# Optimization experiments

Measured on AMD Instinct MI355X. Metric: run time of the kernel, lower is better.

## Reference

```python
import jax, jax.numpy as jnp
import numpy as np

EPS = 1e-5
H = 1024  # hidden_size
IN = 1024  # input_size
B = 4096


def _layer_norm(x, gamma, beta):
    mu = jnp.mean(x, axis=-1, keepdims=True)
    var = jnp.mean(jnp.square(x - mu), axis=-1, keepdims=True)
    return (x - mu) * jax.lax.rsqrt(var + EPS) * gamma + beta


def setup_inputs() -> dict:
    key = jax.random.key(0)
    ks = jax.random.split(key, 8)
    s_h = 1.0 / np.sqrt(H)
    s_x = 1.0 / np.sqrt(IN)
    return {
        "x": jax.random.normal(ks[0], (B, IN), dtype=jnp.float32),
        "h": jax.random.normal(ks[1], (B, H), dtype=jnp.float32),
        "c": jax.random.normal(ks[2], (B, H), dtype=jnp.float32),
        # hidden_lin: Linear(H, 4H) with bias; input_lin: Linear(IN, 4H) no bias
        "W_h": jax.random.uniform(ks[3], (H, 4 * H), jnp.float32, -s_h, s_h),
        "b_h": jax.random.uniform(ks[4], (4 * H,), jnp.float32, -s_h, s_h),
        "W_x": jax.random.uniform(ks[5], (IN, 4 * H), jnp.float32, -s_x, s_x),
        # 4 gate LayerNorms stacked [4,H], plus LayerNorm for c
        "ln_g": jnp.ones((4, H), jnp.float32),
        "ln_b": jnp.zeros((4, H), jnp.float32),
        "lnc_g": jnp.ones((H,), jnp.float32),
        "lnc_b": jnp.zeros((H,), jnp.float32),
    }


def reference(x, h, c, W_h, b_h, W_x, ln_g, ln_b, lnc_g, lnc_b):
    # ifgo = hidden_lin(h) + input_lin(x) : [B, 4H]
    ifgo = h @ W_h + b_h + x @ W_x
    ifgo = ifgo.reshape(x.shape[0], 4, H)  # [B, 4, H]
    ifgo = _layer_norm(ifgo, ln_g, ln_b)   # per-gate LayerNorm over last dim
    i, f, g, o = ifgo[:, 0], ifgo[:, 1], ifgo[:, 2], ifgo[:, 3]
    c_next = jax.nn.sigmoid(f) * c + jax.nn.sigmoid(i) * jnp.tanh(g)
    h_next = jax.nn.sigmoid(o) * jnp.tanh(_layer_norm(c_next, lnc_g, lnc_b))
    return (h_next, c_next)
```

## Files before the change

kernel.cpp:

```cpp
#include <hip/hip_runtime.h>

typedef short bf16x8 __attribute__((ext_vector_type(8)));
typedef unsigned short u16x8 __attribute__((ext_vector_type(8)));
typedef float f32x4  __attribute__((ext_vector_type(4)));

__device__ __forceinline__ float bf2f(unsigned short u) {
  union { unsigned int i; float f; } x; x.i = ((unsigned int)u) << 16; return x.f;
}
__device__ __forceinline__ unsigned short f2bf(float f) {
  union { float f; unsigned int i; } x; x.f = f;
  unsigned int r = x.i + 0x7fffu + ((x.i >> 16) & 1u);
  return (unsigned short)(r >> 16);
}
__device__ __forceinline__ float sigm(float v) { return 1.f / (1.f + __expf(-v)); }
__device__ __forceinline__ float tanh_(float v) { return 1.f - 2.f / (__expf(2.f * v) + 1.f); }
__device__ __forceinline__ int is_fp32(const void* lng) {
  return ((*(const unsigned int*)lng) & 0xFFFFu) == 0u;
}

#define AS1 __attribute__((address_space(1)))
#define AS3 __attribute__((address_space(3)))

__global__ __launch_bounds__(256) void prep_kernel(
    const void* __restrict__ h, const void* __restrict__ x,
    const void* __restrict__ Wh, const void* __restrict__ Wx,
    const void* __restrict__ lng,
    unsigned short* __restrict__ Ap, unsigned short* __restrict__ Wt)
{
  __shared__ unsigned short tile[64][65];
  const int fp = is_fp32(lng);
  if (blockIdx.x < 4096) {
    const int row = blockIdx.x;
    const int col = threadIdx.x * 8;
    const void* src; int sc;
    if (col < 1024) { src = h; sc = col; } else { src = x; sc = col - 1024; }
    u16x8 o;
    if (fp) {
      const float* s = (const float*)src + (size_t)row * 1024 + sc;
      float4 a = *(const float4*)s;
      float4 b = *(const float4*)(s + 4);
      o[0] = f2bf(a.x); o[1] = f2bf(a.y); o[2] = f2bf(a.z); o[3] = f2bf(a.w);
      o[4] = f2bf(b.x); o[5] = f2bf(b.y); o[6] = f2bf(b.z); o[7] = f2bf(b.w);
    } else {
      o = *(const u16x8*)((const unsigned short*)src + (size_t)row * 1024 + sc);
    }
    *(u16x8*)(Ap + (size_t)row * 2048 + col) = o;
  } else {
    const int bid = blockIdx.x - 4096;
    const int n0 = (bid & 63) * 64;
    const int k0 = (bid >> 6) * 64;
    const int tx = threadIdx.x & 63;
    const int ty = threadIdx.x >> 6;
    const void* src; int krow;
    if (k0 < 1024) { src = Wh; krow = k0; } else { src = Wx; krow = k0 - 1024; }
#pragma unroll
    for (int i = 0; i < 16; ++i) {
      int kk = ty + i * 4;
      size_t idx = (size_t)(krow + kk) * 4096 + n0 + tx;
      tile[kk][tx] = fp ? f2bf(((const float*)src)[idx])
                        : ((const unsigned short*)src)[idx];
    }
    __syncthreads();
#pragma unroll
    for (int i = 0; i < 16; ++i) {
      int nn = ty + i * 4;
      Wt[(size_t)(n0 + nn) * 2048 + k0 + tx] = tile[tx][nn];
    }
  }
}

__global__ __launch_bounds__(256) void gemm_kernel(
    const unsigned short* __restrict__ Ap,
    const unsigned short* __restrict__ Wt,
    unsigned short* __restrict__ parts)
{
  __shared__ __align__(16) unsigned short As[128 * 64];
  __shared__ __align__(16) unsigned short Bs[128 * 64];
  const int bn = blockIdx.x, bm = blockIdx.y, kz = blockIdx.z;
  const int tid = threadIdx.x;
  const int wave = tid >> 6, lane = tid & 63;
  const int wm = (wave >> 1) * 64, wn = (wave & 1) * 64;
  const int fr = lane & 15;
  const int fq = lane >> 4;
  const int srow = lane >> 3;
  const int sswz = ((lane & 7) ^ srow) * 8;

  f32x4 acc[4][4] = {};

  const int fbase = fr * 64;
  const int slot0 = ((0 * 4 + fq) ^ (fr & 7)) * 8;
  const int slot1 = ((1 * 4 + fq) ^ (fr & 7)) * 8;

  for (int kt = 0; kt < 16; ++kt) {
    const int kg = kz * 1024 + kt * 64;
    __syncthreads();
#pragma unroll
    for (int i = 0; i < 4; ++i) {
      const int chunk = wave * 4 + i;
      const int row = chunk * 8 + srow;
      const unsigned short* ga = Ap + (size_t)(bm * 128 + row) * 2048 + kg + sswz;
      __builtin_amdgcn_global_load_lds((const AS1 void*)ga,
                                       (AS3 void*)(As + chunk * 512), 16, 0, 0);
      const unsigned short* gb = Wt + (size_t)(bn * 128 + row) * 2048 + kg + sswz;
      __builtin_amdgcn_global_load_lds((const AS1 void*)gb,
                                       (AS3 void*)(Bs + chunk * 512), 16, 0, 0);
    }
    __syncthreads();

#pragma unroll
    for (int kh = 0; kh < 2; ++kh) {
      const int slot = kh ? slot1 : slot0;
      bf16x8 a[4], b[4];
#pragma unroll
      for (int mi = 0; mi < 4; ++mi)
        a[mi] = *(const bf16x8*)(As + (wm + mi * 16) * 64 + fbase + slot);
#pragma unroll
      for (int ni = 0; ni < 4; ++ni)
        b[ni] = *(const bf16x8*)(Bs + (wn + ni * 16) * 64 + fbase + slot);
#pragma unroll
      for (int mi = 0; mi < 4; ++mi)
#pragma unroll
        for (int ni = 0; ni < 4; ++ni)
          acc[mi][ni] = __builtin_amdgcn_mfma_f32_16x16x32_bf16(a[mi], b[ni], acc[mi][ni], 0, 0, 0);
    }
  }

  unsigned short* Cp = parts + (size_t)kz * 4096 * 4096;
#pragma unroll
  for (int mi = 0; mi < 4; ++mi) {
#pragma unroll
    for (int ni = 0; ni < 4; ++ni) {
      const int cm = bm * 128 + wm + mi * 16 + fq * 4;
      const int cn = bn * 128 + wn + ni * 16 + fr;
#pragma unroll
      for (int r = 0; r < 4; ++r)
        Cp[(size_t)(cm + r) * 4096 + cn] = f2bf(acc[mi][ni][r]);
    }
  }
}

__device__ __forceinline__ float4 load4(const void* p, size_t idx, int fp) {
  if (fp) return *(const float4*)((const float*)p + idx);
  ushort4 u = *(const ushort4*)((const unsigned short*)p + idx);
  return make_float4(bf2f(u.x), bf2f(u.y), bf2f(u.z), bf2f(u.w));
}
__device__ __forceinline__ void store4(void* p, size_t idx, int fp,
                                       float a, float b, float c, float d) {
  if (fp) {
    *(float4*)((float*)p + idx) = make_float4(a, b, c, d);
  } else {
    ushort4 u; u.x = f2bf(a); u.y = f2bf(b); u.z = f2bf(c); u.w = f2bf(d);
    *(ushort4*)((unsigned short*)p + idx) = u;
  }
}

__global__ __launch_bounds__(256) void ln_lstm_kernel(
    const unsigned short* __restrict__ parts,
    const void* __restrict__ c,
    const void* __restrict__ bh,
    const void* __restrict__ ln_g,
    const void* __restrict__ ln_b,
    const void* __restrict__ lnc_g,
    const void* __restrict__ lnc_b,
    void* __restrict__ out)
{
  const int b = blockIdx.x;
  const int t = threadIdx.x;
  const int lane = t & 63, wave = t >> 6;
  const int fp = is_fp32(lnc_g);
  const unsigned short* P0 = parts + (size_t)b * 4096;
  const unsigned short* P1 = parts + (size_t)4096 * 4096 + (size_t)b * 4096;

  __shared__ float sred[4][8];

  float v[4][4];
  float red[8];
#pragma unroll
  for (int q = 0; q < 4; ++q) {
    ushort4 p0 = *(const ushort4*)(P0 + q * 1024 + t * 4);
    ushort4 p1 = *(const ushort4*)(P1 + q * 1024 + t * 4);
    float4 b4 = load4(bh, q * 1024 + t * 4, fp);
    v[q][0] = bf2f(p0.x) + bf2f(p1.x) + b4.x;
    v[q][1] = bf2f(p0.y) + bf2f(p1.y) + b4.y;
    v[q][2] = bf2f(p0.z) + bf2f(p1.z) + b4.z;
    v[q][3] = bf2f(p0.w) + bf2f(p1.w) + b4.w;
    red[q * 2]     = v[q][0] + v[q][1] + v[q][2] + v[q][3];
    red[q * 2 + 1] = v[q][0]*v[q][0] + v[q][1]*v[q][1] + v[q][2]*v[q][2] + v[q][3]*v[q][3];
  }
#pragma unroll
  for (int j = 0; j < 8; ++j) {
    float s = red[j];
#pragma unroll
    for (int off = 32; off > 0; off >>= 1) s += __shfl_down(s, off, 64);
    if (lane == 0) sred[wave][j] = s;
  }
  __syncthreads();
  float mu[4], rs[4];
#pragma unroll
  for (int q = 0; q < 4; ++q) {
    float s  = sred[0][2*q]   + sred[1][2*q]   + sred[2][2*q]   + sred[3][2*q];
    float sq = sred[0][2*q+1] + sred[1][2*q+1] + sred[2][2*q+1] + sred[3][2*q+1];
    mu[q] = s * (1.f / 1024.f);
    float var = sq * (1.f / 1024.f) - mu[q] * mu[q];
    rs[q] = rsqrtf(var + 1e-5f);
  }

  float4 gI = load4(ln_g, 0 * 1024 + t * 4, fp), bI = load4(ln_b, 0 * 1024 + t * 4, fp);
  float4 gF = load4(ln_g, 1 * 1024 + t * 4, fp), bF = load4(ln_b, 1 * 1024 + t * 4, fp);
  float4 gG = load4(ln_g, 2 * 1024 + t * 4, fp), bG = load4(ln_b, 2 * 1024 + t * 4, fp);
  float4 gO = load4(ln_g, 3 * 1024 + t * 4, fp), bO = load4(ln_b, 3 * 1024 + t * 4, fp);
  float gg[4][4] = { {gI.x,gI.y,gI.z,gI.w}, {gF.x,gF.y,gF.z,gF.w},
                     {gG.x,gG.y,gG.z,gG.w}, {gO.x,gO.y,gO.z,gO.w} };
  float gb[4][4] = { {bI.x,bI.y,bI.z,bI.w}, {bF.x,bF.y,bF.z,bF.w},
                     {bG.x,bG.y,bG.z,bG.w}, {bO.x,bO.y,bO.z,bO.w} };

  float4 c4 = load4(c, (size_t)b * 1024 + t * 4, fp);
  float cin[4] = { c4.x, c4.y, c4.z, c4.w };

  float cn[4], osg[4];
  float csum = 0.f, csq = 0.f;
#pragma unroll
  for (int e = 0; e < 4; ++e) {
    float iv = (v[0][e] - mu[0]) * rs[0] * gg[0][e] + gb[0][e];
    float fv = (v[1][e] - mu[1]) * rs[1] * gg[1][e] + gb[1][e];
    float gv = (v[2][e] - mu[2]) * rs[2] * gg[2][e] + gb[2][e];
    float ov = (v[3][e] - mu[3]) * rs[3] * gg[3][e] + gb[3][e];
    float cne = sigm(fv) * cin[e] + sigm(iv) * tanh_(gv);
    cn[e] = cne; csum += cne; csq += cne * cne;
    osg[e] = sigm(ov);
  }
  store4(out, (size_t)4096 * 1024 + (size_t)b * 1024 + t * 4, fp, cn[0], cn[1], cn[2], cn[3]);

  __syncthreads();
  {
    float s0 = csum, s1 = csq;
#pragma unroll
    for (int off = 32; off > 0; off >>= 1) { s0 += __shfl_down(s0, off, 64); s1 += __shfl_down(s1, off, 64); }
    if (lane == 0) { sred[wave][0] = s0; sred[wave][1] = s1; }
  }
  __syncthreads();
  float cs   = sred[0][0] + sred[1][0] + sred[2][0] + sred[3][0];
  float csq2 = sred[0][1] + sred[1][1] + sred[2][1] + sred[3][1];
  float mu_c = cs * (1.f / 1024.f);
  float var_c = csq2 * (1.f / 1024.f) - mu_c * mu_c;
  float rs_c = rsqrtf(var_c + 1e-5f);

  float4 cg4 = load4(lnc_g, t * 4, fp);
  float4 cb4 = load4(lnc_b, t * 4, fp);

  float hn[4];
  float cgv[4] = { cg4.x, cg4.y, cg4.z, cg4.w };
  float cbv[4] = { cb4.x, cb4.y, cb4.z, cb4.w };
#pragma unroll
  for (int e = 0; e < 4; ++e)
    hn[e] = osg[e] * tanh_((cn[e] - mu_c) * rs_c * cgv[e] + cbv[e]);
  store4(out, (size_t)b * 1024 + t * 4, fp, hn[0], hn[1], hn[2], hn[3]);
}

extern "C" void kernel_launch(void* const* d_in, const int* in_sizes, int n_in,
                              void* d_out, int out_size, void* d_ws, size_t ws_size,
                              hipStream_t stream) {
  const void* x    = d_in[0];
  const void* h    = d_in[1];
  const void* c    = d_in[2];
  const void* Wh   = d_in[3];
  const void* bh   = d_in[4];
  const void* Wx   = d_in[5];
  const void* lng  = d_in[6];
  const void* lnb  = d_in[7];
  const void* lncg = d_in[8];
  const void* lncb = d_in[9];

  char* ws = (char*)d_ws;
  unsigned short* parts = (unsigned short*)ws;
  unsigned short* Wt    = (unsigned short*)(ws + (size_t)64 * 1024 * 1024);
  unsigned short* Ap    = (unsigned short*)(ws + (size_t)80 * 1024 * 1024);

  prep_kernel<<<6144, 256, 0, stream>>>(h, x, Wh, Wx, lng, Ap, Wt);
  gemm_kernel<<<dim3(32, 32, 2), 256, 0, stream>>>(Ap, Wt, parts);
  ln_lstm_kernel<<<4096, 256, 0, stream>>>(parts, c, bh, lng, lnb, lncg, lncb, d_out);
}
```

Before: 244.2 us.

## Replace split-K GEMM with 256x256 double-buffered pipelined tile kernel

Replaces the 128x128 split-K GEMM with a single-pass kernel that uses 256x256 tiles, 512 threads, double-buffered LDS and interleaved async global-to-LDS staging around MFMA blocks, plus a block-index swizzle. Dropping split-K removes the second bf16 partial buffer and its extra read in the LayerNorm kernel. The intent is higher MFMA utilization through larger tile reuse and overlap of loads with compute. In exchange the grid shrinks to 256 blocks, which may underfill the GPU, and the hand-scheduled barriers and waitcnt logic are fragile.

```diff
diff --git a/kernel.cpp b/kernel.cpp
--- a/kernel.cpp
+++ b/kernel.cpp
@@ -69,74 +69,141 @@
   }
 }
 
-__global__ __launch_bounds__(256) void gemm_kernel(
+
+#define BAR()   __builtin_amdgcn_s_barrier()
+#define SBAR()  __builtin_amdgcn_sched_barrier(0)
+#define LGKM0() { asm volatile("s_waitcnt lgkmcnt(0)" ::: "memory"); SBAR(); }
+#define VMW(N)  { asm volatile("s_waitcnt vmcnt(" #N ")" ::: "memory"); }
+
+#define LOAD_A(DB, MH)                                                         \
+  { const unsigned short* _ba = &As[DB][(MH)*128 + wr*64 + fr][0];             \
+    _Pragma("unroll") for (int mi = 0; mi < 4; ++mi)                           \
+      _Pragma("unroll") for (int kh = 0; kh < 2; ++kh)                         \
+        a[mi][kh] = *(const bf16x8*)(_ba + mi*1024 + ((kh*4 + fq) ^ xk) * 8); }
+
+#define LOAD_B(DB, NH)                                                         \
+  { const unsigned short* _bb = &Bs[DB][(NH)*128 + wc*32 + fr][0];             \
+    _Pragma("unroll") for (int ni = 0; ni < 2; ++ni)                           \
+      _Pragma("unroll") for (int kh = 0; kh < 2; ++kh)                         \
+        b[ni][kh] = *(const bf16x8*)(_bb + ni*1024 + ((kh*4 + fq) ^ xk) * 8); }
+
+#define MFMA16(MH, NH)                                                         \
+  { __builtin_amdgcn_s_setprio(1);                                             \
+    _Pragma("unroll") for (int kh = 0; kh < 2; ++kh)                           \
+      _Pragma("unroll") for (int mi = 0; mi < 4; ++mi)                         \
+        _Pragma("unroll") for (int ni = 0; ni < 2; ++ni)                       \
+          acc[MH][mi][NH][ni] = __builtin_amdgcn_mfma_f32_16x16x32_bf16(       \
+              a[mi][kh], b[ni][kh], acc[MH][mi][NH][ni], 0, 0, 0);             \
+    __builtin_amdgcn_s_setprio(0); }
+
+#define STAGE(G, LDS, ROW0, H, KT)                                             \
+  { _Pragma("unroll") for (int l = 0; l < 2; ++l) {                            \
+      const int _idx = l * 512 + tid;                                          \
+      const int _r = _idx >> 3;                                                \
+      const int _sg = (_idx & 7) ^ (_r & 7);                                   \
+      const unsigned short* _src = (G) + (size_t)((ROW0) + (H)*128 + _r) * 2048\
+                                   + ((KT) << 6) + _sg * 8;                    \
+      __builtin_amdgcn_global_load_lds((const AS1 void*)_src,                  \
+          (AS3 void*)(&(LDS)[0][0] + (H)*8192 + (l*512 + wave*64)*8), 16, 0, 0);\
+  } }
+
+__global__ __launch_bounds__(512, 2) void gemm_kernel(
     const unsigned short* __restrict__ Ap,
     const unsigned short* __restrict__ Wt,
-    unsigned short* __restrict__ parts)
+    unsigned short* __restrict__ Cout)
 {
-  __shared__ __align__(16) unsigned short As[128 * 64];
-  __shared__ __align__(16) unsigned short Bs[128 * 64];
-  const int bn = blockIdx.x, bm = blockIdx.y, kz = blockIdx.z;
-  const int tid = threadIdx.x;
+  __shared__ __align__(16) unsigned short As[2][256][64];
+  __shared__ __align__(16) unsigned short Bs[2][256][64];
+
+  const int bid = blockIdx.x;
+  const int swz = (bid & 7) * 32 + (bid >> 3);
+  const int bm = swz >> 4, bn = swz & 15;
+  const int arow = bm * 256, brow = bn * 256;
+
+  const int tid  = threadIdx.x;
   const int wave = tid >> 6, lane = tid & 63;
-  const int wm = (wave >> 1) * 64, wn = (wave & 1) * 64;
-  const int fr = lane & 15;
-  const int fq = lane >> 4;
-  const int srow = lane >> 3;
-  const int sswz = ((lane & 7) ^ srow) * 8;
-
-  f32x4 acc[4][4] = {};
-
-  const int fbase = fr * 64;
-  const int slot0 = ((0 * 4 + fq) ^ (fr & 7)) * 8;
-  const int slot1 = ((1 * 4 + fq) ^ (fr & 7)) * 8;
-
-  for (int kt = 0; kt < 16; ++kt) {
-    const int kg = kz * 1024 + kt * 64;
-    __syncthreads();
-#pragma unroll
-    for (int i = 0; i < 4; ++i) {
-      const int chunk = wave * 4 + i;
-      const int row = chunk * 8 + srow;
-      const unsigned short* ga = Ap + (size_t)(bm * 128 + row) * 2048 + kg + sswz;
-      __builtin_amdgcn_global_load_lds((const AS1 void*)ga,
-                                       (AS3 void*)(As + chunk * 512), 16, 0, 0);
-      const unsigned short* gb = Wt + (size_t)(bn * 128 + row) * 2048 + kg + sswz;
-      __builtin_amdgcn_global_load_lds((const AS1 void*)gb,
-                                       (AS3 void*)(Bs + chunk * 512), 16, 0, 0);
-    }
-    __syncthreads();
-
-#pragma unroll
-    for (int kh = 0; kh < 2; ++kh) {
-      const int slot = kh ? slot1 : slot0;
-      bf16x8 a[4], b[4];
-#pragma unroll
-      for (int mi = 0; mi < 4; ++mi)
-        a[mi] = *(const bf16x8*)(As + (wm + mi * 16) * 64 + fbase + slot);
-#pragma unroll
-      for (int ni = 0; ni < 4; ++ni)
-        b[ni] = *(const bf16x8*)(Bs + (wn + ni * 16) * 64 + fbase + slot);
-#pragma unroll
-      for (int mi = 0; mi < 4; ++mi)
-#pragma unroll
-        for (int ni = 0; ni < 4; ++ni)
-          acc[mi][ni] = __builtin_amdgcn_mfma_f32_16x16x32_bf16(a[mi], b[ni], acc[mi][ni], 0, 0, 0);
-    }
-  }
-
-  unsigned short* Cp = parts + (size_t)kz * 4096 * 4096;
-#pragma unroll
-  for (int mi = 0; mi < 4; ++mi) {
-#pragma unroll
-    for (int ni = 0; ni < 4; ++ni) {
-      const int cm = bm * 128 + wm + mi * 16 + fq * 4;
-      const int cn = bn * 128 + wn + ni * 16 + fr;
-#pragma unroll
-      for (int r = 0; r < 4; ++r)
-        Cp[(size_t)(cm + r) * 4096 + cn] = f2bf(acc[mi][ni][r]);
-    }
-  }
+  const int wr = wave >> 2, wc = wave & 3;
+  const int fr = lane & 15, fq = lane >> 4;
+  const int xk = fr & 7;
+
+  f32x4 acc[2][4][2][2] = {};
+  bf16x8 a[4][2], b[2][2];
+
+  STAGE(Ap, As[0], arow, 0, 0);
+  STAGE(Ap, As[0], arow, 1, 0);
+  STAGE(Wt, Bs[0], brow, 0, 0);
+  STAGE(Wt, Bs[0], brow, 1, 0);
+  STAGE(Wt, Bs[1], brow, 0, 1);
+  STAGE(Ap, As[1], arow, 1, 1);
+  VMW(4);
+  SBAR(); BAR();
+
+#pragma unroll 1
+  for (int it = 0; it < 16; ++it) {
+    const int t1 = (2 * it + 1) & 31;
+    const int t2 = (2 * it + 2) & 31;
+    const int t3 = (2 * it + 3) & 31;
+
+    LOAD_A(0, 0) LOAD_B(0, 0)
+    STAGE(Ap, As[1], arow, 0, t1);
+    SBAR(); BAR(); LGKM0();
+    MFMA16(0, 0);
+    SBAR(); BAR();
+    LOAD_A(0, 1)
+    STAGE(Wt, Bs[1], brow, 1, t1);
+    SBAR(); BAR(); LGKM0();
+    MFMA16(1, 0);
+    SBAR(); BAR();
+    LOAD_B(0, 1)
+    STAGE(Wt, Bs[0], brow, 0, t2);
+    SBAR(); BAR(); LGKM0();
+    MFMA16(1, 1);
+    SBAR(); BAR();
+    LOAD_A(0, 0)
+    STAGE(Ap, As[0], arow, 1, t2);
+    SBAR(); BAR(); LGKM0();
+    MFMA16(0, 1);
+    VMW(4);
+    SBAR(); BAR();
+    LOAD_A(1, 0) LOAD_B(1, 0)
+    STAGE(Ap, As[0], arow, 0, t2);
+    SBAR(); BAR(); LGKM0();
+    MFMA16(0, 0);
+    SBAR(); BAR();
+    LOAD_A(1, 1)
+    STAGE(Wt, Bs[0], brow, 1, t2);
+    SBAR(); BAR(); LGKM0();
+    MFMA16(1, 0);
+    SBAR(); BAR();
+    LOAD_B(1, 1)
+    STAGE(Wt, Bs[1], brow, 0, t3);
+    SBAR(); BAR(); LGKM0();
+    MFMA16(1, 1);
+    SBAR(); BAR();
+    LOAD_A(1, 0)
+    STAGE(Ap, As[1], arow, 1, t3);
+    SBAR(); BAR(); LGKM0();
+    MFMA16(0, 1);
+    VMW(4);
+    SBAR(); BAR();
+  }
+  VMW(0);
+
+  unsigned short* Cb = Cout + (size_t)arow * 4096 + brow;
+#pragma unroll
+  for (int mh = 0; mh < 2; ++mh)
+#pragma unroll
+    for (int mi = 0; mi < 4; ++mi)
+#pragma unroll
+      for (int nh = 0; nh < 2; ++nh)
+#pragma unroll
+        for (int ni = 0; ni < 2; ++ni) {
+          const int row = mh * 128 + wr * 64 + mi * 16 + fq * 4;
+          const int col = nh * 128 + wc * 32 + ni * 16 + fr;
+#pragma unroll
+          for (int r = 0; r < 4; ++r)
+            Cb[(size_t)(row + r) * 4096 + col] = f2bf(acc[mh][mi][nh][ni][r]);
+        }
 }
 
 __device__ __forceinline__ float4 load4(const void* p, size_t idx, int fp) {
@@ -169,7 +236,6 @@
   const int lane = t & 63, wave = t >> 6;
   const int fp = is_fp32(lnc_g);
   const unsigned short* P0 = parts + (size_t)b * 4096;
-  const unsigned short* P1 = parts + (size_t)4096 * 4096 + (size_t)b * 4096;
 
   __shared__ float sred[4][8];
 
@@ -178,12 +244,11 @@
 #pragma unroll
   for (int q = 0; q < 4; ++q) {
     ushort4 p0 = *(const ushort4*)(P0 + q * 1024 + t * 4);
-    ushort4 p1 = *(const ushort4*)(P1 + q * 1024 + t * 4);
     float4 b4 = load4(bh, q * 1024 + t * 4, fp);
-    v[q][0] = bf2f(p0.x) + bf2f(p1.x) + b4.x;
-    v[q][1] = bf2f(p0.y) + bf2f(p1.y) + b4.y;
-    v[q][2] = bf2f(p0.z) + bf2f(p1.z) + b4.z;
-    v[q][3] = bf2f(p0.w) + bf2f(p1.w) + b4.w;
+    v[q][0] = bf2f(p0.x) + b4.x;
+    v[q][1] = bf2f(p0.y) + b4.y;
+    v[q][2] = bf2f(p0.z) + b4.z;
+    v[q][3] = bf2f(p0.w) + b4.w;
     red[q * 2]     = v[q][0] + v[q][1] + v[q][2] + v[q][3];
     red[q * 2 + 1] = v[q][0]*v[q][0] + v[q][1]*v[q][1] + v[q][2]*v[q][2] + v[q][3]*v[q][3];
   }
@@ -277,6 +342,6 @@
   unsigned short* Ap    = (unsigned short*)(ws + (size_t)80 * 1024 * 1024);
 
   prep_kernel<<<6144, 256, 0, stream>>>(h, x, Wh, Wx, lng, Ap, Wt);
-  gemm_kernel<<<dim3(32, 32, 2), 256, 0, stream>>>(Ap, Wt, parts);
+  gemm_kernel<<<256, 512, 0, stream>>>(Ap, Wt, parts);
   ln_lstm_kernel<<<4096, 256, 0, stream>>>(parts, c, bh, lng, lnb, lncg, lncb, d_out);
 }
```

New measurement: 226.4 us. -7.3%, faster.
